# Kernel tuning notes

Hardware: AMD Instinct MI355X
Metric: run time of the kernel (lower is better)

## Reference

```python
import jax, jax.numpy as jnp
import numpy as np

RATIO = 0.25
R = 0.08            # ball-query radius
K = 32              # max_num_neighbors


def setup_inputs() -> dict:
    key = jax.random.key(0)
    k1, k2 = jax.random.split(key)
    N = 20000
    node_coord_src = jax.random.uniform(k1, (N, 3), dtype=jnp.float32)
    node_feature_src = jax.random.normal(k2, (N, 128), dtype=jnp.float32)
    batch_src = jnp.zeros((N,), dtype=jnp.int32)
    return {"node_coord_src": node_coord_src,
            "node_feature_src": node_feature_src,
            "batch_src": batch_src}


def _fps(coords, n_samples):
    """Farthest point sampling (deterministic start at index 0, random_start=False).
    Returns int32 indices of n_samples points."""
    d0 = jnp.sum((coords - coords[0]) ** 2, axis=-1)  # [N]

    def step(min_d, _):
        nxt = jnp.argmax(min_d)                       # farthest point so far
        d = jnp.sum((coords - coords[nxt]) ** 2, axis=-1)
        return jnp.minimum(min_d, d), nxt

    _, rest = jax.lax.scan(step, d0, None, length=n_samples - 1)
    return jnp.concatenate([jnp.zeros((1,), jnp.int32), rest.astype(jnp.int32)])


def reference(node_coord_src, node_feature_src, batch_src):
    N = node_coord_src.shape[0]
    n_dst = int(RATIO * N)

    # --- FPS (index selection only; non-differentiable in the original) ---
    coords = jax.lax.stop_gradient(node_coord_src)
    idx = _fps(coords, n_dst)                 # [n_dst]
    node_coord_dst = node_coord_src[idx]      # [n_dst, 3]
    batch_dst = batch_src[idx]

    # --- radius (ball query): up to K src neighbors per dst, in src-index order ---
    dst = coords[idx]
    # squared distances via GEMM to avoid materializing [n_dst, N, 3]
    d2 = (jnp.sum(dst ** 2, -1)[:, None] + jnp.sum(coords ** 2, -1)[None, :]
          - 2.0 * dst @ coords.T)             # [n_dst, N]
    within = d2 <= R * R
    # sort key = src index if within radius else N; first K sorted keys are the
    # first K in-radius src indices (matches torch_cluster radius ordering)
    keys = jnp.where(within, jnp.arange(N, dtype=jnp.int32)[None, :], N)
    sorted_keys = jnp.sort(keys, axis=1)[:, :K]   # [n_dst, K]
    valid = sorted_keys < N                       # [n_dst, K]
    nbr = jnp.where(valid, sorted_keys, 0)

    # degree = number of edges per dst node (scatter_add of ones)
    degree = valid.sum(axis=1).astype(jnp.int32)  # [n_dst]

    # scatter_mean of gathered src features onto dst nodes
    feats = node_feature_src[nbr] * valid[..., None].astype(node_feature_src.dtype)
    node_feature_dst = feats.sum(axis=1) / jnp.maximum(degree, 1)[:, None].astype(node_feature_src.dtype)

    # padded edge lists (-1 = no edge); flattened [n_dst * K]
    edge_src = jnp.where(valid, sorted_keys, -1).reshape(-1)
    edge_dst = jnp.where(valid, jnp.arange(n_dst, dtype=jnp.int32)[:, None], -1).reshape(-1)

    return node_coord_dst, node_feature_dst, edge_src, edge_dst, degree, batch_dst
```

## Files before the change

### kernel.cpp

```cpp
#include <hip/hip_runtime.h>

#define KNBR 32
#define NCELL 4096
#define MAXCHUNK 320
#define FCAP (MAXCHUNK * 64)
#define FT 768
#define NWAVE (FT / 64)
#define NSLOT 27
#define NP 14

typedef unsigned long long u64;
typedef unsigned int u32;
typedef float f32x2 __attribute__((ext_vector_type(2)));

__device__ __forceinline__ float sq_dist_nofma(float px, float py, float pz,
                                               float cx, float cy, float cz) {
    float dx = __fsub_rn(px, cx);
    float dy = __fsub_rn(py, cy);
    float dz = __fsub_rn(pz, cz);
    return __fadd_rn(__fadd_rn(__fmul_rn(dx, dx), __fmul_rn(dy, dy)), __fmul_rn(dz, dz));
}

__device__ __forceinline__ unsigned spread4(unsigned v) {
    return (v & 1u) | ((v & 2u) << 2) | ((v & 4u) << 4) | ((v & 8u) << 6);
}

__device__ __forceinline__ u64 pack_key(float md, int orig, int c) {
    return (orig != 0x7fffffff)
        ? (((u64)__float_as_uint(md) << 24) | ((u64)(0x7FFFu - (u32)orig) << 9) | (u64)c)
        : 0ull;
}

template<int CTRL, int RM>
__device__ __forceinline__ u32 dppmax_step(u32 v) {
    u32 t = (u32)__builtin_amdgcn_update_dpp(0, (int)v, CTRL, RM, 0xf, false);
    return t > v ? t : v;
}
__device__ __forceinline__ u32 wave_max_u32(u32 v) {
    v = dppmax_step<0x111, 0xf>(v);
    v = dppmax_step<0x112, 0xf>(v);
    v = dppmax_step<0x114, 0xf>(v);
    v = dppmax_step<0x118, 0xf>(v);
    v = dppmax_step<0x142, 0xa>(v);
    v = dppmax_step<0x143, 0xc>(v);
    return (u32)__builtin_amdgcn_readlane((int)v, 63);
}
__device__ __forceinline__ u32 row16_max_u32(u32 v) {
    v = dppmax_step<0x111, 0xf>(v);
    v = dppmax_step<0x112, 0xf>(v);
    v = dppmax_step<0x114, 0xf>(v);
    v = dppmax_step<0x118, 0xf>(v);
    return (u32)__builtin_amdgcn_readlane((int)v, 15);
}

__global__ void prep_kernel(const float* __restrict__ coord, int N,
                            float* __restrict__ sx, float* __restrict__ sy,
                            float* __restrict__ sz, float* __restrict__ sn,
                            int* __restrict__ cell, int* __restrict__ rank,
                            int* __restrict__ hist) {
    int i = blockIdx.x * blockDim.x + threadIdx.x;
    if (i < N) {
        float x = coord[3 * i + 0];
        float y = coord[3 * i + 1];
        float z = coord[3 * i + 2];
        sx[i] = x; sy[i] = y; sz[i] = z;
        sn[i] = __fadd_rn(__fadd_rn(__fmul_rn(x, x), __fmul_rn(y, y)), __fmul_rn(z, z));
        int ix = (int)(x * 16.0f); ix = ix < 0 ? 0 : (ix > 15 ? 15 : ix);
        int iy = (int)(y * 16.0f); iy = iy < 0 ? 0 : (iy > 15 ? 15 : iy);
        int iz = (int)(z * 16.0f); iz = iz < 0 ? 0 : (iz > 15 ? 15 : iz);
        unsigned mc = spread4(ix) | (spread4(iy) << 1) | (spread4(iz) << 2);
        cell[i] = (int)mc;
        rank[i] = atomicAdd(&hist[mc], 1);
    }
}

__global__ __launch_bounds__(1024) void scan_kernel(const int* __restrict__ hist,
                                                    int* __restrict__ cellstart) {
    __shared__ int buf[1024];
    int t = threadIdx.x;
    int h0 = hist[4 * t], h1 = hist[4 * t + 1], h2 = hist[4 * t + 2], h3 = hist[4 * t + 3];
    int s = h0 + h1 + h2 + h3;
    buf[t] = s;
    __syncthreads();
    for (int off = 1; off < 1024; off <<= 1) {
        int v = (t >= off) ? buf[t - off] : 0;
        __syncthreads();
        buf[t] += v;
        __syncthreads();
    }
    int ex = buf[t] - s;
    cellstart[4 * t]     = ex;
    cellstart[4 * t + 1] = ex + h0;
    cellstart[4 * t + 2] = ex + h0 + h1;
    cellstart[4 * t + 3] = ex + h0 + h1 + h2;
}

__global__ void scatter_kernel(const float* __restrict__ sx, const float* __restrict__ sy,
                               const float* __restrict__ sz,
                               const int* __restrict__ cell, const int* __restrict__ rank,
                               const int* __restrict__ cellstart, int N,
                               float4* __restrict__ pts) {
    int i = blockIdx.x * blockDim.x + threadIdx.x;
    if (i < N) {
        int pos = cellstart[cell[i]] + rank[i];
        pts[pos] = make_float4(sx[i], sy[i], sz[i], __int_as_float(i));
    }
}

__global__ void pad_kernel(float4* __restrict__ pts, int N, int cap) {
    int i = N + blockIdx.x * blockDim.x + threadIdx.x;
    if (i < cap) pts[i] = make_float4(1e18f, 1e18f, 1e18f, __int_as_float(0x7fffffff));
}

__global__ void init_chunk_kernel(const float4* __restrict__ pts,
                                  const float* __restrict__ coord,
                                  float* __restrict__ mdbuf,
                                  float4* __restrict__ spheres,
                                  u64* __restrict__ ckeys,
                                  float4* __restrict__ wxyz_g) {
    int c = blockIdx.x, lane = threadIdx.x;
    int pos = (c << 6) + lane;
    float4 P = pts[pos];
    int orig = __float_as_int(P.w);
    bool real = (orig != 0x7fffffff);
    float c0x = coord[0], c0y = coord[1], c0z = coord[2];
    float d = sq_dist_nofma(P.x, P.y, P.z, c0x, c0y, c0z);
    float m = real ? d : -3e38f;
    mdbuf[pos] = m;
    u64 kself = pack_key(m, orig, c);
    u64 key = kself;
    float mnx = real ? P.x : 1e30f, mxx = real ? P.x : -1e30f;
    float mny = real ? P.y : 1e30f, mxy = real ? P.y : -1e30f;
    float mnz = real ? P.z : 1e30f, mxz = real ? P.z : -1e30f;
    #pragma unroll
    for (int off = 32; off; off >>= 1) {
        u64 k2 = __shfl_xor(key, off, 64);
        if (k2 > key) key = k2;
        mnx = fminf(mnx, __shfl_xor(mnx, off, 64));
        mxx = fmaxf(mxx, __shfl_xor(mxx, off, 64));
        mny = fminf(mny, __shfl_xor(mny, off, 64));
        mxy = fmaxf(mxy, __shfl_xor(mxy, off, 64));
        mnz = fminf(mnz, __shfl_xor(mnz, off, 64));
        mxz = fmaxf(mxz, __shfl_xor(mxz, off, 64));
    }
    if (kself == key) wxyz_g[c] = make_float4(P.x, P.y, P.z, 0.f);
    if (lane == 0) {
        float cx = 0.5f * (mnx + mxx), cy = 0.5f * (mny + mxy), cz = 0.5f * (mnz + mxz);
        float ex = (mxx - mnx) * 0.5f, ey = (mxy - mny) * 0.5f, ez = (mxz - mnz) * 0.5f;
        float r = sqrtf(ex * ex + ey * ey + ez * ez) * 1.0001f + 1e-7f;
        spheres[c] = make_float4(cx, cy, cz, r);
        ckeys[c] = key;
    }
}

__global__ __launch_bounds__(FT, 3)
void fps_kernel(const float4* __restrict__ pts,
                const float* __restrict__ coord,
                const float4* __restrict__ spheres_g, const u64* __restrict__ ckeys_g,
                const float4* __restrict__ wxyz_g,
                int nchunk, int n_dst, int* __restrict__ out_idx) {
#pragma clang fp contract(off)
    __shared__ u64    wwin[2][16];
    __shared__ float4 wcoord[2][NWAVE];

    const int tid = threadIdx.x, lane = tid & 63, wv = tid / 64;
    const int myc = lane * NWAVE + wv;

    const float c0x = coord[0], c0y = coord[1], c0z = coord[2];

    f32x2 px2[NP], py2[NP], pz2[NP], md2[NP];
    u32   po16[NP];
    #pragma unroll
    for (int i = 0; i < NP; ++i) {
        px2[i] = (f32x2)(0.f); py2[i] = (f32x2)(0.f);
        pz2[i] = (f32x2)(0.f); md2[i] = (f32x2)(0.f);
        po16[i] = 0xFFFFFFFFu;
    }
    #pragma unroll
    for (int r = 0; r < NSLOT; ++r) {
        int c = r * NWAVE + wv;
        float x = 0.f, y = 0.f, z = 0.f, md = 0.f;
        u32 o = 0xFFFFu;
        if (c < nchunk) {
            float4 P = pts[(c << 6) + lane];
            int orig = __float_as_int(P.w);
            x = P.x; y = P.y; z = P.z;
            if (orig != 0x7fffffff) {
                o = (u32)orig;
                md = sq_dist_nofma(x, y, z, c0x, c0y, c0z);
            }
        }
        const int i = r >> 1;
        if (r & 1) { px2[i].y = x; py2[i].y = y; pz2[i].y = z; md2[i].y = md;
                     po16[i] = (po16[i] & 0x0000FFFFu) | (o << 16); }
        else       { px2[i].x = x; py2[i].x = y; pz2[i].x = z; md2[i].x = md;
                     po16[i] = (po16[i] & 0xFFFF0000u) | o; }
    }

    u64 k0 = 0ull;
    float wx = 0.f, wy = 0.f, wz = 0.f;
    int wlane = 0;
    float4 S = make_float4(1e18f, 1e18f, 1e18f, 0.f);
    if (lane < NSLOT && myc < nchunk) {
        k0 = ckeys_g[myc];
        float4 W = wxyz_g[myc];
        wx = W.x; wy = W.y; wz = W.z;
        S = spheres_g[myc];
    }
    #pragma unroll
    for (int r = 0; r < NSLOT; ++r) {
        u32 lov = (u32)__builtin_amdgcn_readlane((int)(u32)k0, r) & 0xFFFFFFu;
        u32 o = (po16[r >> 1] >> (16 * (r & 1))) & 0xFFFFu;
        u32 pl = ((0x7FFFu - o) << 9) | (u32)(r * NWAVE + wv);
        u64 mk = __ballot(o != 0xFFFFu && pl == lov);
        if (lane == r && mk) wlane = __ffsll(mk) - 1;
    }

    if (tid == 0) out_idx[0] = 0;
    if (tid < 16) { wwin[0][tid] = 0ull; wwin[1][tid] = 0ull; }
    __syncthreads();

    int par = 1;
    for (int s = 1; s < n_dst; ++s) {
        u32 hi  = (u32)(k0 >> 32);
        u32 mhi = wave_max_u32(hi);
        u64 tbA = __ballot(hi == mhi);
        u32 mlo;
        if (__popcll(tbA) == 1) {
            mlo = (u32)__builtin_amdgcn_readlane((int)(u32)k0,
                                                 (int)(__ffsll((long long)tbA) - 1));
        } else {
            mlo = wave_max_u32(hi == mhi ? (u32)k0 : 0u);
        }
        u64 k = ((u64)mhi << 32) | mlo;
        if (k0 == k && k0 != 0ull) {
            wwin[par][wv]   = k;
            wcoord[par][wv] = make_float4(wx, wy, wz, 0.f);
        }
        float thr = -1.0f;
        if (k0 != 0ull) {
            float maxmd = __uint_as_float((u32)(k0 >> 24));
            float t0 = sqrtf(maxmd) * 1.0001f + S.w;
            thr = t0 * t0 * 1.0002f + 1e-12f;
        }
        __syncthreads();

        u64 wval = wwin[par][lane & 15];
        u32 shi = (u32)(wval >> 32), slo = (u32)wval;
        u32 mhiS = row16_max_u32(shi);
        u64 tbS = __ballot((lane < 16) && shi == mhiS);
        u32 mloS; int wb;
        if (__popcll(tbS) == 1) {
            wb = (int)(__ffsll((long long)tbS) - 1);
            mloS = (u32)__builtin_amdgcn_readlane((int)slo, wb);
        } else {
            mloS = row16_max_u32((shi == mhiS && lane < 16) ? slo : 0u);
            wb = (int)(__ffsll((long long)__ballot((lane < 16) && shi == mhiS
                                                   && slo == mloS)) - 1);
        }
        u64 kb = ((u64)mhiS << 32) | mloS;
        float4 C4 = wcoord[par][wb];
        float ncx = C4.x, ncy = C4.y, ncz = C4.z;
        if (tid == 0) out_idx[s] = (int)(0x7FFFu - (u32)((kb >> 9) & 0x7FFFull));
        par ^= 1;

        bool act = false;
        if (k0 != 0ull) {
            float Dx = ncx - S.x, Dy = ncy - S.y, Dz = ncz - S.z;
            float D2 = Dx * Dx + Dy * Dy + Dz * Dz;
            act = (D2 <= thr);
        }
        u64 m = __ballot(act);

        f32x2 nx2; nx2.x = ncx; nx2.y = ncx;
        f32x2 ny2; ny2.x = ncy; ny2.y = ncy;
        f32x2 nz2; nz2.x = ncz; nz2.y = ncz;
        #pragma unroll
        for (int i = 0; i < NP; ++i) {
            if ((m >> (2 * i)) & 3ull) {
                f32x2 dx = px2[i] - nx2;
                f32x2 dy = py2[i] - ny2;
                f32x2 dz = pz2[i] - nz2;
                f32x2 dd = (dx * dx + dy * dy) + dz * dz;
                bool ca = dd.x < md2[i].x;
                bool cb = dd.y < md2[i].y;
                u64 mca = __ballot(ca);
                u64 mcb = __ballot(cb);
                md2[i].x = ca ? dd.x : md2[i].x;
                md2[i].y = cb ? dd.y : md2[i].y;
                #pragma unroll
                for (int h = 0; h < 2; ++h) {
                    const int r = 2 * i + h;
                    u64 mchg = h ? mcb : mca;
                    if (mchg) {
                        int wlo = __builtin_amdgcn_readlane(wlane, r);
                        if ((mchg >> wlo) & 1ull) {
                            float pm = h ? md2[i].y : md2[i].x;
                            u32 v  = __float_as_uint(pm);
                            u32 mv = wave_max_u32(v);
                            u64 tb = __ballot(v == mv);
                            int wl; u32 low;
                            if (__popcll(tb) == 1) {
                                wl = (int)(__ffsll((long long)tb) - 1);
                                u32 pw = (u32)__builtin_amdgcn_readlane((int)po16[i], wl);
                                u32 ow = (pw >> (16 * h)) & 0xFFFFu;
                                low = ((0x7FFFu - ow) << 9) | (u32)(r * NWAVE + wv);
                            } else {
                                u32 o2 = (po16[i] >> (16 * h)) & 0xFFFFu;
                                u32 pl = (v == mv && o2 != 0xFFFFu)
                                       ? (((0x7FFFu - o2) << 9) | (u32)(r * NWAVE + wv)) : 0u;
                                u32 t2 = wave_max_u32(pl);
                                wl = (int)(__ffsll((long long)__ballot(pl == t2 && pl != 0u)) - 1);
                                low = t2;
                            }
                            float sxr = h ? px2[i].y : px2[i].x;
                            float syr = h ? py2[i].y : py2[i].x;
                            float szr = h ? pz2[i].y : pz2[i].x;
                            float bx = __uint_as_float((u32)__builtin_amdgcn_readlane(__float_as_int(sxr), wl));
                            float by = __uint_as_float((u32)__builtin_amdgcn_readlane(__float_as_int(syr), wl));
                            float bz = __uint_as_float((u32)__builtin_amdgcn_readlane(__float_as_int(szr), wl));
                            if (lane == r) {
                                k0 = ((u64)mv << 24) | low;
                                wx = bx; wy = by; wz = bz; wlane = wl;
                            }
                        }
                    }
                }
            }
        }
    }
}

__global__ void ball_kernel(const float* __restrict__ sx, const float* __restrict__ sy,
                            const float* __restrict__ sz, const float* __restrict__ sn,
                            const int* __restrict__ idx,
                            const float* __restrict__ coord, const int* __restrict__ batch,
                            int N, int n_dst,
                            float* __restrict__ out_coord, float* __restrict__ out_esrc,
                            float* __restrict__ out_edst, float* __restrict__ out_deg,
                            float* __restrict__ out_batch,
                            int* __restrict__ nbr_i, int* __restrict__ deg_i) {
    const int d    = blockIdx.x;
    const int lane = threadIdx.x;
    __shared__ int nbr[KNBR];

    const int id = idx[d];
    const float cx = sx[id], cy = sy[id], cz = sz[id];
    const float dn = sn[id];
    const float RR = (float)(0.08 * 0.08);

    int cnt = 0;
    for (int base = 0; base < N && cnt < KNBR; base += 64) {
        int i = base + lane;
        bool in = false;
        if (i < N) {
            float t     = __fmul_rn(sx[i], cx);
            float inner = __fmaf_rn(sy[i], cy, t);
            inner       = __fmaf_rn(sz[i], cz, inner);
            float d2    = __fsub_rn(__fadd_rn(dn, sn[i]), __fmul_rn(2.0f, inner));
            in = (d2 <= RR);
        }
        unsigned long long m = __ballot(in);
        int pos = cnt + __popcll(m & ((1ull << lane) - 1ull));
        if (in && pos < KNBR) nbr[pos] = i;
        cnt += (int)__popcll(m);
    }
    __syncthreads();

    int deg = cnt < KNBR ? cnt : KNBR;
    if (lane < KNBR) {
        int e = (lane < deg) ? nbr[lane] : -1;
        out_esrc[d * KNBR + lane] = (float)e;
        out_edst[d * KNBR + lane] = (float)((lane < deg) ? d : -1);
        nbr_i[d * KNBR + lane] = e;
    }
    if (lane == 0) { out_deg[d] = (float)deg; deg_i[d] = deg; }
    if (lane < 3)  out_coord[d * 3 + lane] = coord[id * 3 + lane];
    if (lane == 3) out_batch[d] = (float)batch[id];
}

__global__ void agg_kernel(const float* __restrict__ feat,
                           const int* __restrict__ nbr_i, const int* __restrict__ deg_i,
                           int F, float* __restrict__ out_feat) {
    const int d = blockIdx.x;
    const int t = threadIdx.x;
    const int deg = deg_i[d];
    float acc = 0.0f;
    for (int k = 0; k < deg; ++k) {
        int nb = nbr_i[d * KNBR + k];
        acc = __fadd_rn(acc, feat[nb * F + t]);
    }
    float den = (float)(deg > 0 ? deg : 1);
    out_feat[d * F + t] = acc / den;
}

extern "C" void kernel_launch(void* const* d_in, const int* in_sizes, int n_in,
                              void* d_out, int out_size, void* d_ws, size_t ws_size,
                              hipStream_t stream) {
    const float* coord = (const float*)d_in[0];
    const float* feat  = (const float*)d_in[1];
    const int*   batch = (const int*)d_in[2];

    const int N      = in_sizes[0] / 3;
    const int F      = in_sizes[1] / N;
    const int n_dst  = N / 4;
    const int nchunk = (N + 63) / 64;

    float*  sx      = (float*)d_ws;
    float*  sy      = sx + N;
    float*  sz      = sy + N;
    float*  sn      = sz + N;
    float4* pts     = (float4*)(sn + N);
    float4* spheres = pts + FCAP;
    float4* wxyz_g  = spheres + MAXCHUNK;
    float*  mdbuf   = (float*)(wxyz_g + MAXCHUNK);
    u64*    ckeys   = (u64*)(mdbuf + FCAP);
    int*    cell      = (int*)(ckeys + MAXCHUNK);
    int*    rank      = cell + N;
    int*    hist      = rank + N;
    int*    cellstart = hist + NCELL;
    int*    idx       = cellstart + NCELL;
    int*    nbr_i     = idx + n_dst;
    int*    deg_i     = nbr_i + n_dst * KNBR;

    float* out     = (float*)d_out;
    float* o_coord = out;
    float* o_feat  = o_coord + (size_t)n_dst * 3;
    float* o_esrc  = o_feat  + (size_t)n_dst * F;
    float* o_edst  = o_esrc  + (size_t)n_dst * KNBR;
    float* o_deg   = o_edst  + (size_t)n_dst * KNBR;
    float* o_batch = o_deg   + n_dst;

    hipMemsetAsync(hist, 0, NCELL * sizeof(int), stream);
    prep_kernel<<<(N + 255) / 256, 256, 0, stream>>>(coord, N, sx, sy, sz, sn,
                                                     cell, rank, hist);
    scan_kernel<<<1, 1024, 0, stream>>>(hist, cellstart);
    scatter_kernel<<<(N + 255) / 256, 256, 0, stream>>>(sx, sy, sz, cell, rank,
                                                        cellstart, N, pts);
    pad_kernel<<<(nchunk * 64 - N + 255) / 256, 256, 0, stream>>>(pts, N, nchunk * 64);
    init_chunk_kernel<<<nchunk, 64, 0, stream>>>(pts, coord, mdbuf, spheres, ckeys,
                                                 wxyz_g);
    fps_kernel<<<1, FT, 0, stream>>>(pts, coord, spheres, ckeys, wxyz_g,
                                     nchunk, n_dst, idx);
    ball_kernel<<<n_dst, 64, 0, stream>>>(sx, sy, sz, sn, idx, coord, batch, N, n_dst,
                                          o_coord, o_esrc, o_edst, o_deg, o_batch,
                                          nbr_i, deg_i);
    agg_kernel<<<n_dst, F, 0, stream>>>(feat, nbr_i, deg_i, F, o_feat);
}
```

Measured before the change: 5.191 ms.

## Defer per-wave argmax to lazy group rescans and bound chunks by decaying upper bounds

Per-chunk exact max keys and winner tracking are removed from the FPS kernel. Each wave now keeps per-lane, per-group best candidates, rescanned only for groups whose min-distances changed, and does one wave-wide argmax per step. Chunk pruning now uses a conservative upper bound that is lowered by factors of two via ballots, instead of the exact chunk max. This cuts the many per-slot wave reductions inside the update loop, but the bound is looser and may let more chunks through the pruning test, and the output index decoding changes to match the new key packing.

```diff
diff --git a/kernel.cpp b/kernel.cpp
--- a/kernel.cpp
+++ b/kernel.cpp
@@ -8,6 +8,7 @@
 #define NWAVE (FT / 64)
 #define NSLOT 27
 #define NP 14
+#define NG 4
 
 typedef unsigned long long u64;
 typedef unsigned int u32;
@@ -51,6 +52,16 @@
     v = dppmax_step<0x114, 0xf>(v);
     v = dppmax_step<0x118, 0xf>(v);
     return (u32)__builtin_amdgcn_readlane((int)v, 15);
+}
+
+__device__ __forceinline__ void take5(bool t, u32& bh, u32& bl, float& bx, float& by, float& bz,
+                                      u32 nh, u32 nl, float nx, float ny, float nz) {
+    bh = t ? nh : bh; bl = t ? nl : bl;
+    bx = t ? nx : bx; by = t ? ny : by; bz = t ? nz : bz;
+}
+
+__device__ __forceinline__ float readlane_f(float v, int l) {
+    return __uint_as_float((u32)__builtin_amdgcn_readlane(__float_as_int(v), l));
 }
 
 __global__ void prep_kernel(const float* __restrict__ coord, int N,
@@ -157,7 +168,6 @@
 void fps_kernel(const float4* __restrict__ pts,
                 const float* __restrict__ coord,
                 const float4* __restrict__ spheres_g, const u64* __restrict__ ckeys_g,
-                const float4* __restrict__ wxyz_g,
                 int nchunk, int n_dst, int* __restrict__ out_idx) {
 #pragma clang fp contract(off)
     __shared__ u64    wwin[2][16];
@@ -169,52 +179,48 @@
     const float c0x = coord[0], c0y = coord[1], c0z = coord[2];
 
     f32x2 px2[NP], py2[NP], pz2[NP], md2[NP];
-    u32   po16[NP];
+    u32   po[NP];
     #pragma unroll
     for (int i = 0; i < NP; ++i) {
         px2[i] = (f32x2)(0.f); py2[i] = (f32x2)(0.f);
         pz2[i] = (f32x2)(0.f); md2[i] = (f32x2)(0.f);
-        po16[i] = 0xFFFFFFFFu;
+        po[i] = 0u;
     }
     #pragma unroll
     for (int r = 0; r < NSLOT; ++r) {
         int c = r * NWAVE + wv;
         float x = 0.f, y = 0.f, z = 0.f, md = 0.f;
-        u32 o = 0xFFFFu;
+        u32 ss = 0u;
         if (c < nchunk) {
             float4 P = pts[(c << 6) + lane];
             int orig = __float_as_int(P.w);
             x = P.x; y = P.y; z = P.z;
             if (orig != 0x7fffffff) {
-                o = (u32)orig;
+                ss = 0x7FFFu - (u32)orig;
                 md = sq_dist_nofma(x, y, z, c0x, c0y, c0z);
             }
         }
         const int i = r >> 1;
         if (r & 1) { px2[i].y = x; py2[i].y = y; pz2[i].y = z; md2[i].y = md;
-                     po16[i] = (po16[i] & 0x0000FFFFu) | (o << 16); }
+                     po[i] |= (ss << 16); }
         else       { px2[i].x = x; py2[i].x = y; pz2[i].x = z; md2[i].x = md;
-                     po16[i] = (po16[i] & 0xFFFF0000u) | o; }
-    }
-
-    u64 k0 = 0ull;
-    float wx = 0.f, wy = 0.f, wz = 0.f;
-    int wlane = 0;
+                     po[i] |= ss; }
+    }
+
+    bool  has = (lane < NSLOT) && (myc < nchunk);
+    float ub = 0.f;
     float4 S = make_float4(1e18f, 1e18f, 1e18f, 0.f);
-    if (lane < NSLOT && myc < nchunk) {
-        k0 = ckeys_g[myc];
-        float4 W = wxyz_g[myc];
-        wx = W.x; wy = W.y; wz = W.z;
+    if (has) {
+        ub = __uint_as_float((u32)(ckeys_g[myc] >> 24));
         S = spheres_g[myc];
     }
+
+    u32 gh[NG], gl[NG]; float gx[NG], gy[NG], gz[NG];
+    u64 accg[NG];
     #pragma unroll
-    for (int r = 0; r < NSLOT; ++r) {
-        u32 lov = (u32)__builtin_amdgcn_readlane((int)(u32)k0, r) & 0xFFFFFFu;
-        u32 o = (po16[r >> 1] >> (16 * (r & 1))) & 0xFFFFu;
-        u32 pl = ((0x7FFFu - o) << 9) | (u32)(r * NWAVE + wv);
-        u64 mk = __ballot(o != 0xFFFFu && pl == lov);
-        if (lane == r && mk) wlane = __ffsll(mk) - 1;
-    }
+    for (int g = 0; g < NG; ++g) { gh[g] = 0; gl[g] = 0; gx[g] = gy[g] = gz[g] = 0.f;
+                                   accg[g] = ~0ull; }
+    u64 ck = 0ull; float cwx = 0.f, cwy = 0.f, cwz = 0.f;
 
     if (tid == 0) out_idx[0] = 0;
     if (tid < 16) { wwin[0][tid] = 0ull; wwin[1][tid] = 0ull; }
@@ -222,25 +228,55 @@
 
     int par = 1;
     for (int s = 1; s < n_dst; ++s) {
-        u32 hi  = (u32)(k0 >> 32);
-        u32 mhi = wave_max_u32(hi);
-        u64 tbA = __ballot(hi == mhi);
-        u32 mlo;
-        if (__popcll(tbA) == 1) {
-            mlo = (u32)__builtin_amdgcn_readlane((int)(u32)k0,
-                                                 (int)(__ffsll((long long)tbA) - 1));
-        } else {
-            mlo = wave_max_u32(hi == mhi ? (u32)k0 : 0u);
-        }
-        u64 k = ((u64)mhi << 32) | mlo;
-        if (k0 == k && k0 != 0ull) {
-            wwin[par][wv]   = k;
-            wcoord[par][wv] = make_float4(wx, wy, wz, 0.f);
+        u64 af = accg[0] | accg[1] | accg[2] | accg[3];
+        if (af) {
+            #pragma unroll
+            for (int g = 0; g < NG; ++g) {
+                if (accg[g]) {
+                    accg[g] = 0ull;
+                    const int r0 = g * 8;
+                    const int r1 = (g == NG - 1) ? NSLOT : (r0 + 8);
+                    u32 bh = 0, bl = 0; float bx = 0.f, by = 0.f, bz = 0.f;
+                    #pragma unroll
+                    for (int r = r0; r < r1; ++r) {
+                        const int i = r >> 1, h = r & 1;
+                        u32 nh  = __float_as_uint(h ? md2[i].y : md2[i].x);
+                        u32 nl  = (po[i] >> (16 * h)) & 0xFFFFu;
+                        float nx = h ? px2[i].y : px2[i].x;
+                        float ny = h ? py2[i].y : py2[i].x;
+                        float nz = h ? pz2[i].y : pz2[i].x;
+                        bool t = (nh > bh) || (nh == bh && nl > bl);
+                        take5(t, bh, bl, bx, by, bz, nh, nl, nx, ny, nz);
+                    }
+                    gh[g] = bh; gl[g] = bl; gx[g] = bx; gy[g] = by; gz[g] = bz;
+                }
+            }
+            u32 whi = gh[0], wlo = gl[0]; float wx = gx[0], wy = gy[0], wz = gz[0];
+            #pragma unroll
+            for (int g = 1; g < NG; ++g) {
+                bool t = (gh[g] > whi) || (gh[g] == whi && gl[g] > wlo);
+                take5(t, whi, wlo, wx, wy, wz, gh[g], gl[g], gx[g], gy[g], gz[g]);
+            }
+            u32 mhi = wave_max_u32(whi);
+            u64 tbA = __ballot(whi == mhi);
+            u32 mlo; int wl;
+            if (__popcll(tbA) == 1) {
+                wl = (int)(__ffsll((long long)tbA) - 1);
+                mlo = (u32)__builtin_amdgcn_readlane((int)wlo, wl);
+            } else {
+                mlo = wave_max_u32(whi == mhi ? wlo : 0u);
+                wl = (int)(__ffsll((long long)__ballot(whi == mhi && wlo == mlo)) - 1);
+            }
+            ck = ((u64)mhi << 32) | mlo;
+            cwx = readlane_f(wx, wl); cwy = readlane_f(wy, wl); cwz = readlane_f(wz, wl);
+        }
+        if (lane == 0) {
+            wwin[par][wv]   = ck;
+            wcoord[par][wv] = make_float4(cwx, cwy, cwz, 0.f);
         }
         float thr = -1.0f;
-        if (k0 != 0ull) {
-            float maxmd = __uint_as_float((u32)(k0 >> 24));
-            float t0 = sqrtf(maxmd) * 1.0001f + S.w;
+        if (has) {
+            float t0 = sqrtf(ub) * 1.0001f + S.w;
             thr = t0 * t0 * 1.0002f + 1e-12f;
         }
         __syncthreads();
@@ -261,11 +297,11 @@
         u64 kb = ((u64)mhiS << 32) | mloS;
         float4 C4 = wcoord[par][wb];
         float ncx = C4.x, ncy = C4.y, ncz = C4.z;
-        if (tid == 0) out_idx[s] = (int)(0x7FFFu - (u32)((kb >> 9) & 0x7FFFull));
+        if (tid == 0) out_idx[s] = (int)(0x7FFFu - (u32)(kb & 0x7FFFull));
         par ^= 1;
 
         bool act = false;
-        if (k0 != 0ull) {
+        if (has) {
             float Dx = ncx - S.x, Dy = ncy - S.y, Dz = ncz - S.z;
             float D2 = Dx * Dx + Dy * Dy + Dz * Dz;
             act = (D2 <= thr);
@@ -286,43 +322,20 @@
                 bool cb = dd.y < md2[i].y;
                 u64 mca = __ballot(ca);
                 u64 mcb = __ballot(cb);
+                accg[i >> 2] |= mca | mcb;
                 md2[i].x = ca ? dd.x : md2[i].x;
                 md2[i].y = cb ? dd.y : md2[i].y;
                 #pragma unroll
                 for (int h = 0; h < 2; ++h) {
                     const int r = 2 * i + h;
-                    u64 mchg = h ? mcb : mca;
-                    if (mchg) {
-                        int wlo = __builtin_amdgcn_readlane(wlane, r);
-                        if ((mchg >> wlo) & 1ull) {
-                            float pm = h ? md2[i].y : md2[i].x;
-                            u32 v  = __float_as_uint(pm);
-                            u32 mv = wave_max_u32(v);
-                            u64 tb = __ballot(v == mv);
-                            int wl; u32 low;
-                            if (__popcll(tb) == 1) {
-                                wl = (int)(__ffsll((long long)tb) - 1);
-                                u32 pw = (u32)__builtin_amdgcn_readlane((int)po16[i], wl);
-                                u32 ow = (pw >> (16 * h)) & 0xFFFFu;
-                                low = ((0x7FFFu - ow) << 9) | (u32)(r * NWAVE + wv);
-                            } else {
-                                u32 o2 = (po16[i] >> (16 * h)) & 0xFFFFu;
-                                u32 pl = (v == mv && o2 != 0xFFFFu)
-                                       ? (((0x7FFFu - o2) << 9) | (u32)(r * NWAVE + wv)) : 0u;
-                                u32 t2 = wave_max_u32(pl);
-                                wl = (int)(__ffsll((long long)__ballot(pl == t2 && pl != 0u)) - 1);
-                                low = t2;
-                            }
-                            float sxr = h ? px2[i].y : px2[i].x;
-                            float syr = h ? py2[i].y : py2[i].x;
-                            float szr = h ? pz2[i].y : pz2[i].x;
-                            float bx = __uint_as_float((u32)__builtin_amdgcn_readlane(__float_as_int(sxr), wl));
-                            float by = __uint_as_float((u32)__builtin_amdgcn_readlane(__float_as_int(syr), wl));
-                            float bz = __uint_as_float((u32)__builtin_amdgcn_readlane(__float_as_int(szr), wl));
-                            if (lane == r) {
-                                k0 = ((u64)mv << 24) | low;
-                                wx = bx; wy = by; wz = bz; wlane = wl;
-                            }
+                    if ((m >> r) & 1ull) {
+                        float ubb = readlane_f(ub, r);
+                        float mdv = h ? md2[i].y : md2[i].x;
+                        u64 b2 = __ballot(mdv >= 0.50f * ubb);
+                        u64 b4 = __ballot(mdv >= 0.25f * ubb);
+                        if (lane == r) {
+                            if (!b4)      ub *= 0.25f;
+                            else if (!b2) ub *= 0.50f;
                         }
                     }
                 }
@@ -440,7 +453,7 @@
     pad_kernel<<<(nchunk * 64 - N + 255) / 256, 256, 0, stream>>>(pts, N, nchunk * 64);
     init_chunk_kernel<<<nchunk, 64, 0, stream>>>(pts, coord, mdbuf, spheres, ckeys,
                                                  wxyz_g);
-    fps_kernel<<<1, FT, 0, stream>>>(pts, coord, spheres, ckeys, wxyz_g,
+    fps_kernel<<<1, FT, 0, stream>>>(pts, coord, spheres, ckeys,
                                      nchunk, n_dst, idx);
     ball_kernel<<<n_dst, 64, 0, stream>>>(sx, sy, sz, sn, idx, coord, batch, N, n_dst,
                                           o_coord, o_esrc, o_edst, o_deg, o_batch,
```

New measurement: 9.477 ms. 82.6% more time.
